# Performance work log

Hardware: AMD Instinct MI355X
Metric: run time of the kernel (lower is better)

Reference implementation:

```python
import jax, jax.numpy as jnp
import numpy as np

SEQ, BATCH, HID, NLAYERS = 2048, 16, 1024, 2


def setup_inputs() -> dict:
    key = jax.random.key(0)
    ks = jax.random.split(key, 3)
    scale = 1.0 / np.sqrt(HID)
    x = jax.random.normal(ks[0], (SEQ, BATCH, HID), dtype=jnp.float32)
    W0 = jax.random.normal(ks[1], (HID, 3 * HID), dtype=jnp.float32) * scale
    b0 = jnp.zeros((2 * HID,), dtype=jnp.float32)
    W1 = jax.random.normal(ks[2], (HID, 3 * HID), dtype=jnp.float32) * scale
    b1 = jnp.zeros((2 * HID,), dtype=jnp.float32)
    return {"x": x, "W0": W0, "b0": b0, "W1": W1, "b1": b1}


def _sru_layer(x, W, b):
    # x: [L, B, H]; W: [H, 3H]; b: [2H]
    L, B, H = x.shape
    U = jnp.einsum('lbd,dk->lbk', x, W)  # [L, B, 3H]
    x_tilde = U[..., :H]
    bf, br = b[:H], b[H:]
    f = jax.nn.sigmoid(U[..., H:2 * H] + bf)  # forget gate [L,B,H]
    r = jax.nn.sigmoid(U[..., 2 * H:] + br)   # reset gate  [L,B,H]

    def step(c_prev, inp):
        xt_t, f_t = inp
        c_t = f_t * c_prev + (1.0 - f_t) * xt_t
        return c_t, c_t

    c0 = jnp.zeros((B, H), dtype=x.dtype)
    _, cs = jax.lax.scan(step, c0, (x_tilde, f))  # cs: [L, B, H]
    h = r * cs + (1.0 - r) * x  # highway connection
    return h


def reference(x, W0, b0, W1, b1):
    h = _sru_layer(x, W0, b0)
    h = _sru_layer(h, W1, b1)
    return h[-1:]  # [1, B, H], matching `out[-1:]`
```

## Files before the change

kernel.cpp:

```cpp
#include <hip/hip_runtime.h>

#define SEQ    2048
#define BATCH  16
#define HID    1024
#define M_TOT  (SEQ*BATCH)
#define NCH    (BATCH*HID)
#define NCHUNK 64
#define TCHUNK (SEQ/NCHUNK)
#define NSEG   128

typedef __attribute__((ext_vector_type(8))) short          short8;
typedef __attribute__((ext_vector_type(8))) unsigned short ushort8_t;
typedef __attribute__((ext_vector_type(4))) float          floatx4;

__device__ __forceinline__ unsigned short f32_to_bf16(float f) {
  unsigned int u = __float_as_uint(f);
  u += 0x7FFFu + ((u >> 16) & 1u);
  return (unsigned short)(u >> 16);
}
__device__ __forceinline__ float bf16_to_f32(unsigned short h) {
  return __uint_as_float(((unsigned int)h) << 16);
}
__device__ __forceinline__ float sigmoidf_(float x) {
  return 1.f / (1.f + __expf(-x));
}


__device__ __forceinline__ void cast_swizzle_body(const float* __restrict__ src,
    unsigned short* __restrict__ dst, int mt, int kt, int t) {
  __shared__ unsigned short tile[4096];
  const int r = t >> 1, kh = (t & 1) * 16;
  const float* sp = src + (size_t)(mt * 128 + r) * 1024 + kt * 32 + kh;
  float4 v0 = *(const float4*)(sp + 0);
  float4 v1 = *(const float4*)(sp + 4);
  float4 v2 = *(const float4*)(sp + 8);
  float4 v3 = *(const float4*)(sp + 12);
  ushort8_t u0, u1;
  u0[0]=f32_to_bf16(v0.x); u0[1]=f32_to_bf16(v0.y); u0[2]=f32_to_bf16(v0.z); u0[3]=f32_to_bf16(v0.w);
  u0[4]=f32_to_bf16(v1.x); u0[5]=f32_to_bf16(v1.y); u0[6]=f32_to_bf16(v1.z); u0[7]=f32_to_bf16(v1.w);
  u1[0]=f32_to_bf16(v2.x); u1[1]=f32_to_bf16(v2.y); u1[2]=f32_to_bf16(v2.z); u1[3]=f32_to_bf16(v2.w);
  u1[4]=f32_to_bf16(v3.x); u1[5]=f32_to_bf16(v3.y); u1[6]=f32_to_bf16(v3.z); u1[7]=f32_to_bf16(v3.w);
  const int c = r >> 4, lr = r & 15, q0 = kh >> 3;
  const int unit0 = c * 64 + (q0 << 4) + lr;
  *(ushort8_t*)&tile[unit0 * 8]        = u0;
  *(ushort8_t*)&tile[(unit0 + 16) * 8] = u1;
  __syncthreads();
  const size_t base = ((size_t)mt * 32 + kt) * 4096;
  *(ushort8_t*)&dst[base + t * 16]     = *(const ushort8_t*)&tile[t * 16];
  *(ushort8_t*)&dst[base + t * 16 + 8] = *(const ushort8_t*)&tile[t * 16 + 8];
}

__device__ __forceinline__ void w_prep_body(const float* __restrict__ W,
    unsigned short* __restrict__ Wsw, int nt, int kt, int t) {
  __shared__ unsigned short tile[4096];
  const int kk = t >> 3, n0 = (t & 7) * 16;
  const float* sp = W + (size_t)(kt * 32 + kk) * 3072 + nt * 128 + n0;
  float v[16];
#pragma unroll
  for (int i = 0; i < 16; i += 4) {
    float4 f = *(const float4*)(sp + i);
    v[i] = f.x; v[i+1] = f.y; v[i+2] = f.z; v[i+3] = f.w;
  }
  const int cbase = (n0 >> 4) * 64 + ((kk >> 3) << 4);
#pragma unroll
  for (int j = 0; j < 16; j++)
    tile[(cbase + j) * 8 + (kk & 7)] = f32_to_bf16(v[j]);
  __syncthreads();
  const size_t base = ((size_t)nt * 32 + kt) * 4096;
  *(ushort8_t*)&Wsw[base + t * 16]     = *(const ushort8_t*)&tile[t * 16];
  *(ushort8_t*)&Wsw[base + t * 16 + 8] = *(const ushort8_t*)&tile[t * 16 + 8];
}

__global__ __launch_bounds__(256) void prep_all(const float* __restrict__ x,
    const float* __restrict__ W0, const float* __restrict__ W1,
    unsigned short* __restrict__ xsw, unsigned short* __restrict__ W0sw,
    unsigned short* __restrict__ W1sw) {
  const int id = blockIdx.x, t = threadIdx.x;
  if (id < 8192)        cast_swizzle_body(x, xsw, id >> 5, id & 31, t);
  else if (id < 8960)   w_prep_body(W0, W0sw, (id - 8192) >> 5, (id - 8192) & 31, t);
  else                  w_prep_body(W1, W1sw, (id - 8960) >> 5, (id - 8960) & 31, t);
}

typedef __attribute__((address_space(1))) const unsigned int GUI;
typedef __attribute__((address_space(3))) unsigned int LUI;
__device__ __forceinline__ void gl16(const unsigned short* g, unsigned short* l) {
  __builtin_amdgcn_global_load_lds((GUI*)g, (LUI*)l, 16, 0, 0);
}
__device__ __forceinline__ void barrier_fence() {
  asm volatile("s_barrier" ::: "memory");
}

__global__ __launch_bounds__(512, 2) void gemm_pipe(
    const unsigned short* __restrict__ A, const unsigned short* __restrict__ B,
    unsigned short* __restrict__ Xt, unsigned short* __restrict__ Fo,
    unsigned short* __restrict__ Ro, const float* __restrict__ bias)
{
  __shared__ unsigned short lds[65536];
  const int tid = threadIdx.x;
  const int wave = tid >> 6, lane = tid & 63;
  const int wm = wave >> 2, wn = wave & 3;
  const int id = blockIdx.x;
  const int xcd = id & 7, slot = id >> 3;
  const int g = slot / 96, r = slot % 96;
  const int bn = r >> 3;
  const int bm = xcd * 16 + g * 8 + (r & 7);

  const unsigned short* aSrc0 = A + ((size_t)(2 * bm + 0) * 32) * 4096 + tid * 8;
  const unsigned short* aSrc1 = A + ((size_t)(2 * bm + 1) * 32) * 4096 + tid * 8;
  const unsigned short* bSrc0 = B + ((size_t)(2 * bn + 0) * 32) * 4096 + tid * 8;
  const unsigned short* bSrc1 = B + ((size_t)(2 * bn + 1) * 32) * 4096 + tid * 8;

  floatx4 acc[8][4];
#pragma unroll
  for (int i = 0; i < 8; i++)
#pragma unroll
    for (int j = 0; j < 4; j++)
#pragma unroll
      for (int rr = 0; rr < 4; rr++) acc[i][j][rr] = 0.f;

#pragma unroll
  for (int u = 0; u < 3; ++u) {
    unsigned short* d = &lds[u * 16384 + wave * 512];
    gl16(aSrc0 + (size_t)u * 4096, d);
    gl16(aSrc1 + (size_t)u * 4096, d + 4096);
    gl16(bSrc0 + (size_t)u * 4096, d + 8192);
    gl16(bSrc1 + (size_t)u * 4096, d + 12288);
  }
  asm volatile("s_waitcnt vmcnt(0)" ::: "memory");
  barrier_fence();

  const int aoff = wm * 4096 + lane * 8;
  const int boff = 8192 + (wn >> 1) * 4096 + (wn & 1) * 2048 + lane * 8;

#pragma unroll 1
  for (int t = 0; t < 32; ++t) {
    const int sb = (t & 3) * 16384;
    const int u = t + 3;
    const unsigned short* As = &lds[sb + aoff];
    const unsigned short* Bs = &lds[sb + boff];
    short8 br[4], ar[4];
#pragma unroll
    for (int nj = 0; nj < 4; ++nj) br[nj] = *(const short8*)(Bs + nj * 512);
#pragma unroll
    for (int mi = 0; mi < 4; ++mi) ar[mi] = *(const short8*)(As + mi * 512);
    if (u < 32) {
      unsigned short* d = &lds[(u & 3) * 16384 + wave * 512];
      gl16(aSrc0 + (size_t)u * 4096, d);
      gl16(aSrc1 + (size_t)u * 4096, d + 4096);
    }
    __builtin_amdgcn_s_setprio(1);
#pragma unroll
    for (int mi = 0; mi < 4; ++mi)
#pragma unroll
      for (int nj = 0; nj < 4; ++nj)
        acc[mi][nj] = __builtin_amdgcn_mfma_f32_16x16x32_bf16(ar[mi], br[nj], acc[mi][nj], 0, 0, 0);
    __builtin_amdgcn_s_setprio(0);
#pragma unroll
    for (int mi = 0; mi < 4; ++mi) ar[mi] = *(const short8*)(As + (4 + mi) * 512);
    if (u < 32) {
      unsigned short* d = &lds[(u & 3) * 16384 + wave * 512];
      gl16(bSrc0 + (size_t)u * 4096, d + 8192);
      gl16(bSrc1 + (size_t)u * 4096, d + 12288);
    }
    __builtin_amdgcn_s_setprio(1);
#pragma unroll
    for (int mi = 0; mi < 4; ++mi)
#pragma unroll
      for (int nj = 0; nj < 4; ++nj)
        acc[4 + mi][nj] = __builtin_amdgcn_mfma_f32_16x16x32_bf16(ar[mi], br[nj], acc[4 + mi][nj], 0, 0, 0);
    __builtin_amdgcn_s_setprio(0);
    if (t <= 28)      asm volatile("s_waitcnt vmcnt(8)" ::: "memory");
    else if (t == 29) asm volatile("s_waitcnt vmcnt(4)" ::: "memory");
    else if (t == 30) asm volatile("s_waitcnt vmcnt(0)" ::: "memory");
    barrier_fence();
  }

  const int region = bn >> 2;
  const int cc = lane & 15, q = lane >> 4;
  const int lc0 = (bn & 3) * 256 + wn * 64 + cc;
  const int row0 = bm * 256 + wm * 128 + q * 4;
  if (region == 0) {
#pragma unroll
    for (int mi = 0; mi < 8; ++mi)
#pragma unroll
      for (int rg = 0; rg < 4; ++rg)
#pragma unroll
        for (int nj = 0; nj < 4; ++nj)
          Xt[(size_t)(row0 + mi * 16 + rg) * 1024 + lc0 + nj * 16] =
              f32_to_bf16(acc[mi][nj][rg]);
  } else {
    unsigned short* O = (region == 1) ? Fo : Ro;
    const float* bp = bias + (region - 1) * 1024;
    float bb[4];
#pragma unroll
    for (int nj = 0; nj < 4; ++nj) bb[nj] = bp[lc0 + nj * 16];
#pragma unroll
    for (int mi = 0; mi < 8; ++mi)
#pragma unroll
      for (int rg = 0; rg < 4; ++rg)
#pragma unroll
        for (int nj = 0; nj < 4; ++nj) {
          float s = sigmoidf_(acc[mi][nj][rg] + bb[nj]);
          O[(size_t)(row0 + mi * 16 + rg) * 1024 + lc0 + nj * 16] = f32_to_bf16(s);
        }
  }
}

__global__ __launch_bounds__(512, 2) void gemm2_scan(
    const unsigned short* __restrict__ A, const unsigned short* __restrict__ B,
    const float* __restrict__ bias, float* __restrict__ Pseg, float* __restrict__ Sseg)
{
  __shared__ unsigned short lds[65536];
  const int tid = threadIdx.x;
  const int wave = tid >> 6, lane = tid & 63;
  const int wm = wave >> 2, wn = wave & 3;
  const int id = blockIdx.x;
  const int xcd = id & 7, slot = id >> 3;
  const int bn = slot >> 4;
  const int bm = xcd * 16 + (slot & 15);

  const unsigned short* aSrc0 = A + ((size_t)(2 * bm + 0) * 32) * 4096 + tid * 8;
  const unsigned short* aSrc1 = A + ((size_t)(2 * bm + 1) * 32) * 4096 + tid * 8;
  const unsigned short* bxSrc = B + ((size_t)bn * 32) * 4096 + tid * 8;
  const unsigned short* bfSrc = B + ((size_t)(8 + bn) * 32) * 4096 + tid * 8;

  floatx4 ax[8][2], af[8][2];
#pragma unroll
  for (int i = 0; i < 8; i++)
#pragma unroll
    for (int j = 0; j < 2; j++)
#pragma unroll
      for (int rr = 0; rr < 4; rr++) { ax[i][j][rr] = 0.f; af[i][j][rr] = 0.f; }

#pragma unroll
  for (int u = 0; u < 3; ++u) {
    unsigned short* d = &lds[u * 16384 + wave * 512];
    gl16(aSrc0 + (size_t)u * 4096, d);
    gl16(aSrc1 + (size_t)u * 4096, d + 4096);
    gl16(bxSrc + (size_t)u * 4096, d + 8192);
    gl16(bfSrc + (size_t)u * 4096, d + 12288);
  }
  asm volatile("s_waitcnt vmcnt(0)" ::: "memory");
  barrier_fence();

  const int aoff  = wm * 4096 + lane * 8;
  const int bxoff = 8192  + wn * 1024 + lane * 8;
  const int bfoff = 12288 + wn * 1024 + lane * 8;

#pragma unroll 1
  for (int t = 0; t < 32; ++t) {
    const int sb = (t & 3) * 16384;
    const int u = t + 3;
    const unsigned short* As  = &lds[sb + aoff];
    const unsigned short* Bxs = &lds[sb + bxoff];
    const unsigned short* Bfs = &lds[sb + bfoff];
    short8 bx[2], bf[2], ar[4];
#pragma unroll
    for (int nj = 0; nj < 2; ++nj) {
      bx[nj] = *(const short8*)(Bxs + nj * 512);
      bf[nj] = *(const short8*)(Bfs + nj * 512);
    }
#pragma unroll
    for (int mi = 0; mi < 4; ++mi) ar[mi] = *(const short8*)(As + mi * 512);
    if (u < 32) {
      unsigned short* d = &lds[(u & 3) * 16384 + wave * 512];
      gl16(aSrc0 + (size_t)u * 4096, d);
      gl16(aSrc1 + (size_t)u * 4096, d + 4096);
    }
    __builtin_amdgcn_s_setprio(1);
#pragma unroll
    for (int mi = 0; mi < 4; ++mi)
#pragma unroll
      for (int nj = 0; nj < 2; ++nj) {
        ax[mi][nj] = __builtin_amdgcn_mfma_f32_16x16x32_bf16(ar[mi], bx[nj], ax[mi][nj], 0, 0, 0);
        af[mi][nj] = __builtin_amdgcn_mfma_f32_16x16x32_bf16(ar[mi], bf[nj], af[mi][nj], 0, 0, 0);
      }
    __builtin_amdgcn_s_setprio(0);
#pragma unroll
    for (int mi = 0; mi < 4; ++mi) ar[mi] = *(const short8*)(As + (4 + mi) * 512);
    if (u < 32) {
      unsigned short* d = &lds[(u & 3) * 16384 + wave * 512];
      gl16(bxSrc + (size_t)u * 4096, d + 8192);
      gl16(bfSrc + (size_t)u * 4096, d + 12288);
    }
    __builtin_amdgcn_s_setprio(1);
#pragma unroll
    for (int mi = 0; mi < 4; ++mi)
#pragma unroll
      for (int nj = 0; nj < 2; ++nj) {
        ax[4 + mi][nj] = __builtin_amdgcn_mfma_f32_16x16x32_bf16(ar[mi], bx[nj], ax[4 + mi][nj], 0, 0, 0);
        af[4 + mi][nj] = __builtin_amdgcn_mfma_f32_16x16x32_bf16(ar[mi], bf[nj], af[4 + mi][nj], 0, 0, 0);
      }
    __builtin_amdgcn_s_setprio(0);
    if (t <= 28)      asm volatile("s_waitcnt vmcnt(8)" ::: "memory");
    else if (t == 29) asm volatile("s_waitcnt vmcnt(4)" ::: "memory");
    else if (t == 30) asm volatile("s_waitcnt vmcnt(0)" ::: "memory");
    barrier_fence();
  }

  const int q = lane >> 4, cc = lane & 15;
  float pv[2][4], sv[2][4];
#pragma unroll
  for (int nj = 0; nj < 2; ++nj) {
    float bb = bias[bn * 128 + wn * 32 + nj * 16 + cc];
#pragma unroll
    for (int rg = 0; rg < 4; ++rg) {
      float p = 1.f, s = 0.f;
#pragma unroll
      for (int mi = 0; mi < 8; ++mi) {
        float f  = sigmoidf_(af[mi][nj][rg] + bb);
        float xt = ax[mi][nj][rg];
        s = f * s + (1.f - f) * xt;
        p *= f;
      }
      pv[nj][rg] = p; sv[nj][rg] = s;
    }
  }
  float* lf = (float*)lds;
  __syncthreads();
  if (wm == 0) {
#pragma unroll
    for (int nj = 0; nj < 2; ++nj)
#pragma unroll
      for (int rg = 0; rg < 4; ++rg) {
        const int idx = (((wn * 64 + lane) * 4 + rg) * 2 + nj) * 2;
        lf[idx]     = pv[nj][rg];
        lf[idx + 1] = sv[nj][rg];
      }
  }
  __syncthreads();
  if (wm == 1) {
#pragma unroll
    for (int nj = 0; nj < 2; ++nj) {
      const int h = bn * 128 + wn * 32 + nj * 16 + cc;
#pragma unroll
      for (int rg = 0; rg < 4; ++rg) {
        const int idx = (((wn * 64 + lane) * 4 + rg) * 2 + nj) * 2;
        float plo = lf[idx], slo = lf[idx + 1];
        float phi = pv[nj][rg], shi = sv[nj][rg];
        const size_t off = (size_t)bm * NCH + (q * 4 + rg) * 1024 + h;
        Pseg[off] = plo * phi;
        Sseg[off] = phi * slo + shi;
      }
    }
  }
}

__global__ __launch_bounds__(256) void scan_pass1(
    const unsigned short* __restrict__ Xt, const unsigned short* __restrict__ F,
    float* __restrict__ P, float* __restrict__ S) {
  const int ch = (blockIdx.x * 256 + threadIdx.x) * 8;
  const int chunk = blockIdx.y;
  size_t idx = (size_t)chunk * TCHUNK * NCH + ch;
  float p[8], s[8];
#pragma unroll
  for (int j = 0; j < 8; j++) { p[j] = 1.f; s[j] = 0.f; }
  for (int t = 0; t < TCHUNK; ++t) {
    ushort8_t fv = *(const ushort8_t*)&F[idx];
    ushort8_t xv = *(const ushort8_t*)&Xt[idx];
#pragma unroll
    for (int j = 0; j < 8; j++) {
      float f  = bf16_to_f32(fv[j]);
      float xt = bf16_to_f32(xv[j]);
      s[j] = f * s[j] + (1.f - f) * xt;
      p[j] *= f;
    }
    idx += NCH;
  }
  float4* P4 = (float4*)&P[(size_t)chunk * NCH + ch];
  float4* S4 = (float4*)&S[(size_t)chunk * NCH + ch];
  P4[0] = make_float4(p[0], p[1], p[2], p[3]);
  P4[1] = make_float4(p[4], p[5], p[6], p[7]);
  S4[0] = make_float4(s[0], s[1], s[2], s[3]);
  S4[1] = make_float4(s[4], s[5], s[6], s[7]);
}

__global__ __launch_bounds__(256) void combine_c0(
    const float* __restrict__ P, const float* __restrict__ S, float* __restrict__ C0) {
  const int ch = blockIdx.x * 256 + threadIdx.x;
  float c = 0.f;
#pragma unroll 4
  for (int k = 0; k < NCHUNK; ++k) {
    C0[(size_t)k * NCH + ch] = c;
    c = P[(size_t)k * NCH + ch] * c + S[(size_t)k * NCH + ch];
  }
}

#define TPAD 4112
__global__ __launch_bounds__(256) void scan1_pass2_fused(
    const unsigned short* __restrict__ Xt, const unsigned short* __restrict__ F,
    const unsigned short* __restrict__ R, unsigned short* __restrict__ xsw,
    const float* __restrict__ C0, unsigned short* __restrict__ h1last)
{
  __shared__ unsigned short st[4 * TPAD];
  const int hb = blockIdx.x;
  const int chunk = blockIdx.y;
  const int tid = threadIdx.x;
  const int b = tid >> 4, hg = tid & 15;
  const int h0 = hb * 128 + hg * 8;
  const int ch = b * 1024 + h0;
  const int tl   = hg >> 2;
  const int usub = (hg & 3) * 16 + b;

  float c[8];
  {
    const float4* C4 = (const float4*)&C0[(size_t)chunk * NCH + ch];
    float4 a = C4[0], d = C4[1];
    c[0]=a.x; c[1]=a.y; c[2]=a.z; c[3]=a.w; c[4]=d.x; c[5]=d.y; c[6]=d.z; c[7]=d.w;
  }

  size_t idx = (size_t)chunk * TCHUNK * NCH + ch;
  for (int t8 = 0; t8 < TCHUNK / 8; ++t8) {
#pragma unroll
    for (int ts = 0; ts < 8; ++ts) {
      const int t = chunk * TCHUNK + t8 * 8 + ts;
      ushort8_t fv = *(const ushort8_t*)&F[idx];
      ushort8_t xv = *(const ushort8_t*)&Xt[idx];
      ushort8_t rv = *(const ushort8_t*)&R[idx];
      const size_t soff = ((size_t)(t >> 3) * 32 + (h0 >> 5)) * 4096
                        + (size_t)(((t & 7) * 64 + usub) * 8);
      ushort8_t xo = *(const ushort8_t*)&xsw[soff];
      ushort8_t hv;
#pragma unroll
      for (int j = 0; j < 8; ++j) {
        float f  = bf16_to_f32(fv[j]);
        float xt = bf16_to_f32(xv[j]);
        c[j] = f * c[j] + (1.f - f) * xt;
        float r  = bf16_to_f32(rv[j]);
        float xval = bf16_to_f32(xo[j]);
        hv[j] = f32_to_bf16(r * c[j] + (1.f - r) * xval);
      }
      *(ushort8_t*)&st[tl * TPAD + (ts * 64 + usub) * 8] = hv;
      if (t == SEQ - 1) *(ushort8_t*)&h1last[ch] = hv;
      idx += NCH;
    }
    __syncthreads();
    const size_t gbase = (((size_t)chunk * (TCHUNK / 8) + t8) * 32 + hb * 4) * 4096;
#pragma unroll
    for (int tl2 = 0; tl2 < 4; ++tl2) {
      size_t gdst = gbase + (size_t)tl2 * 4096 + tid * 16;
      *(ushort8_t*)&xsw[gdst]     = *(const ushort8_t*)&st[tl2 * TPAD + tid * 16];
      *(ushort8_t*)&xsw[gdst + 8] = *(const ushort8_t*)&st[tl2 * TPAD + tid * 16 + 8];
    }
    __syncthreads();
  }
}

__global__ __launch_bounds__(256) void final_l2(
    const float* __restrict__ Pseg, const float* __restrict__ Sseg,
    const unsigned short* __restrict__ h1last, const float* __restrict__ W1,
    const float* __restrict__ b1, float* __restrict__ out) {
  __shared__ float xrow[1024];
  const int ch = blockIdx.x * 256 + threadIdx.x;
  const int b = ch >> 10;
  const int n = ch & 1023;
  for (int i = threadIdx.x; i < 1024; i += 256)
    xrow[i] = bf16_to_f32(h1last[b * 1024 + i]);
  __syncthreads();
  float racc = b1[1024 + n];
  for (int d = 0; d < 1024; ++d)
    racc += xrow[d] * W1[(size_t)d * 3072 + 2048 + n];
  const float r = sigmoidf_(racc);
  float c = 0.f;
#pragma unroll 8
  for (int k = 0; k < NSEG; ++k)
    c = Pseg[(size_t)k * NCH + ch] * c + Sseg[(size_t)k * NCH + ch];
  out[ch] = r * c + (1.f - r) * xrow[n];
}

extern "C" void kernel_launch(void* const* d_in, const int* in_sizes, int n_in,
                              void* d_out, int out_size, void* d_ws, size_t ws_size,
                              hipStream_t stream) {
  const float* x  = (const float*)d_in[0];
  const float* W0 = (const float*)d_in[1];
  const float* b0 = (const float*)d_in[2];
  const float* W1 = (const float*)d_in[3];
  const float* b1 = (const float*)d_in[4];
  float* out = (float*)d_out;

  char* ws = (char*)d_ws;
  auto alloc = [&](size_t bytes) {
    char* p = ws; ws += (bytes + 255) & ~(size_t)255; return p;
  };
  const size_t NE = (size_t)M_TOT * HID;
  unsigned short* xsw   = (unsigned short*)alloc(NE * 2);
  unsigned short* W0sw  = (unsigned short*)alloc((size_t)3072 * 1024 * 2);
  unsigned short* W1sw  = (unsigned short*)alloc((size_t)3072 * 1024 * 2);
  unsigned short* Xt    = (unsigned short*)alloc(NE * 2);
  unsigned short* F     = (unsigned short*)alloc(NE * 2);
  unsigned short* R     = (unsigned short*)alloc(NE * 2);
  unsigned short* h1last= (unsigned short*)alloc((size_t)NCH * 2);
  float* P    = (float*)alloc((size_t)NCHUNK * NCH * 4);
  float* S    = (float*)alloc((size_t)NCHUNK * NCH * 4);
  float* C0   = (float*)alloc((size_t)NCHUNK * NCH * 4);
  float* Pseg = (float*)alloc((size_t)NSEG * NCH * 4);
  float* Sseg = (float*)alloc((size_t)NSEG * NCH * 4);

  dim3 blk256(256);
  prep_all<<<dim3(9728), blk256, 0, stream>>>(x, W0, W1, xsw, W0sw, W1sw);
  gemm_pipe<<<dim3(1536), dim3(512), 0, stream>>>(xsw, W0sw, Xt, F, R, b0);
  scan_pass1<<<dim3(8, NCHUNK), blk256, 0, stream>>>(Xt, F, P, S);
  combine_c0<<<dim3(NCH / 256), blk256, 0, stream>>>(P, S, C0);
  scan1_pass2_fused<<<dim3(8, NCHUNK), blk256, 0, stream>>>(Xt, F, R, xsw, C0, h1last);
  gemm2_scan<<<dim3(1024), dim3(512), 0, stream>>>(xsw, W1sw, b1, Pseg, Sseg);
  final_l2<<<dim3(NCH / 256), blk256, 0, stream>>>(Pseg, Sseg, h1last, W1, b1, out);
}
```

Baseline: 731.2 us.

## Fuse layer-1 scan passes into one cooperative kernel with grid syncs

Merges the three layer-1 chunked-scan kernels (per-chunk pass, carry combine, apply pass) into one cooperative kernel of 512 blocks that uses grid-wide syncs between phases. This removes two kernel launches and their tail gaps. The cost is two grid barriers, with only 64 blocks working during the combine phase, plus the requirement that all 512 blocks be co-resident. Each block uses about 33 KB of shared memory and is declared at two blocks per SM.

```diff
diff --git a/kernel.cpp b/kernel.cpp
--- a/kernel.cpp
+++ b/kernel.cpp
@@ -1,4 +1,6 @@
 #include <hip/hip_runtime.h>
+#include <hip/hip_cooperative_groups.h>
+namespace cg = cooperative_groups;
 
 #define SEQ    2048
 #define BATCH  16
@@ -346,55 +348,18 @@
   }
 }
 
-__global__ __launch_bounds__(256) void scan_pass1(
-    const unsigned short* __restrict__ Xt, const unsigned short* __restrict__ F,
-    float* __restrict__ P, float* __restrict__ S) {
-  const int ch = (blockIdx.x * 256 + threadIdx.x) * 8;
-  const int chunk = blockIdx.y;
-  size_t idx = (size_t)chunk * TCHUNK * NCH + ch;
-  float p[8], s[8];
-#pragma unroll
-  for (int j = 0; j < 8; j++) { p[j] = 1.f; s[j] = 0.f; }
-  for (int t = 0; t < TCHUNK; ++t) {
-    ushort8_t fv = *(const ushort8_t*)&F[idx];
-    ushort8_t xv = *(const ushort8_t*)&Xt[idx];
-#pragma unroll
-    for (int j = 0; j < 8; j++) {
-      float f  = bf16_to_f32(fv[j]);
-      float xt = bf16_to_f32(xv[j]);
-      s[j] = f * s[j] + (1.f - f) * xt;
-      p[j] *= f;
-    }
-    idx += NCH;
-  }
-  float4* P4 = (float4*)&P[(size_t)chunk * NCH + ch];
-  float4* S4 = (float4*)&S[(size_t)chunk * NCH + ch];
-  P4[0] = make_float4(p[0], p[1], p[2], p[3]);
-  P4[1] = make_float4(p[4], p[5], p[6], p[7]);
-  S4[0] = make_float4(s[0], s[1], s[2], s[3]);
-  S4[1] = make_float4(s[4], s[5], s[6], s[7]);
-}
-
-__global__ __launch_bounds__(256) void combine_c0(
-    const float* __restrict__ P, const float* __restrict__ S, float* __restrict__ C0) {
-  const int ch = blockIdx.x * 256 + threadIdx.x;
-  float c = 0.f;
-#pragma unroll 4
-  for (int k = 0; k < NCHUNK; ++k) {
-    C0[(size_t)k * NCH + ch] = c;
-    c = P[(size_t)k * NCH + ch] * c + S[(size_t)k * NCH + ch];
-  }
-}
-
 #define TPAD 4112
-__global__ __launch_bounds__(256) void scan1_pass2_fused(
+__global__ __launch_bounds__(256, 2) void scan_fused(
     const unsigned short* __restrict__ Xt, const unsigned short* __restrict__ F,
     const unsigned short* __restrict__ R, unsigned short* __restrict__ xsw,
-    const float* __restrict__ C0, unsigned short* __restrict__ h1last)
+    float* __restrict__ P, float* __restrict__ S, float* __restrict__ C0,
+    unsigned short* __restrict__ h1last)
 {
+  cg::grid_group grid = cg::this_grid();
   __shared__ unsigned short st[4 * TPAD];
-  const int hb = blockIdx.x;
-  const int chunk = blockIdx.y;
+  const int bid = blockIdx.x;
+  const int hb = bid & 7;
+  const int chunk = bid >> 3;
   const int tid = threadIdx.x;
   const int b = tid >> 4, hg = tid & 15;
   const int h0 = hb * 128 + hg * 8;
@@ -402,13 +367,51 @@
   const int tl   = hg >> 2;
   const int usub = (hg & 3) * 16 + b;
 
+  {
+    size_t idx = (size_t)chunk * TCHUNK * NCH + ch;
+    float p[8], s[8];
+#pragma unroll
+    for (int j = 0; j < 8; j++) { p[j] = 1.f; s[j] = 0.f; }
+    for (int t = 0; t < TCHUNK; ++t) {
+      ushort8_t fv = *(const ushort8_t*)&F[idx];
+      ushort8_t xv = *(const ushort8_t*)&Xt[idx];
+#pragma unroll
+      for (int j = 0; j < 8; j++) {
+        float f  = bf16_to_f32(fv[j]);
+        float xt = bf16_to_f32(xv[j]);
+        s[j] = f * s[j] + (1.f - f) * xt;
+        p[j] *= f;
+      }
+      idx += NCH;
+    }
+    float4* P4 = (float4*)&P[(size_t)chunk * NCH + ch];
+    float4* S4 = (float4*)&S[(size_t)chunk * NCH + ch];
+    P4[0] = make_float4(p[0], p[1], p[2], p[3]);
+    P4[1] = make_float4(p[4], p[5], p[6], p[7]);
+    S4[0] = make_float4(s[0], s[1], s[2], s[3]);
+    S4[1] = make_float4(s[4], s[5], s[6], s[7]);
+  }
+  __threadfence();
+  grid.sync();
+
+  if (bid < 64) {
+    const int ch2 = bid * 256 + tid;
+    float c = 0.f;
+#pragma unroll 4
+    for (int k = 0; k < NCHUNK; ++k) {
+      C0[(size_t)k * NCH + ch2] = c;
+      c = P[(size_t)k * NCH + ch2] * c + S[(size_t)k * NCH + ch2];
+    }
+  }
+  __threadfence();
+  grid.sync();
+
   float c[8];
   {
     const float4* C4 = (const float4*)&C0[(size_t)chunk * NCH + ch];
     float4 a = C4[0], d = C4[1];
     c[0]=a.x; c[1]=a.y; c[2]=a.z; c[3]=a.w; c[4]=d.x; c[5]=d.y; c[6]=d.z; c[7]=d.w;
   }
-
   size_t idx = (size_t)chunk * TCHUNK * NCH + ch;
   for (int t8 = 0; t8 < TCHUNK / 8; ++t8) {
 #pragma unroll
@@ -499,9 +502,12 @@
   dim3 blk256(256);
   prep_all<<<dim3(9728), blk256, 0, stream>>>(x, W0, W1, xsw, W0sw, W1sw);
   gemm_pipe<<<dim3(1536), dim3(512), 0, stream>>>(xsw, W0sw, Xt, F, R, b0);
-  scan_pass1<<<dim3(8, NCHUNK), blk256, 0, stream>>>(Xt, F, P, S);
-  combine_c0<<<dim3(NCH / 256), blk256, 0, stream>>>(P, S, C0);
-  scan1_pass2_fused<<<dim3(8, NCHUNK), blk256, 0, stream>>>(Xt, F, R, xsw, C0, h1last);
+  {
+    void* args[] = {(void*)&Xt, (void*)&F, (void*)&R, (void*)&xsw,
+                    (void*)&P, (void*)&S, (void*)&C0, (void*)&h1last};
+    hipLaunchCooperativeKernel(reinterpret_cast<void*>(scan_fused),
+                               dim3(512), blk256, args, 0, stream);
+  }
   gemm2_scan<<<dim3(1024), dim3(512), 0, stream>>>(xsw, W1sw, b1, Pseg, Sseg);
   final_l2<<<dim3(NCH / 256), blk256, 0, stream>>>(Pseg, Sseg, h1last, W1, b1, out);
 }
```

Result: slower. 960.8 us (+31.4%).
